# Performance work log

Measured on AMD Instinct MI355X. Metric: run time of the kernel, lower is better.

The kernel has to match this reference:

```python
import jax, jax.numpy as jnp
import numpy as np

STRIDE = (1, 1)
PADDING = ((1, 1), (1, 1))  # symmetric padding of 1 on H and W
DILATION = (1, 1)


def setup_inputs() -> dict:
    key = jax.random.key(0)
    k1, k2 = jax.random.split(key)
    x = jax.random.normal(k1, (32, 128, 56, 56), dtype=jnp.float32)
    weight = jax.random.normal(k2, (256, 128, 3, 3), dtype=jnp.float32) * 0.05
    return {"x": x, "weight": weight}


def reference(x, weight):
    # Faithful math of the im2col + matmul conv: identical to a standard
    # cross-correlation Conv2d with stride=1, padding=1, dilation=1, groups=1,
    # bias=False. Expressed as a single fused conv instead of the python-loop
    # gather + stacked GEMM of the original (same output values).
    out = jax.lax.conv_general_dilated(
        x, weight,
        window_strides=STRIDE,
        padding=PADDING,
        rhs_dilation=DILATION,
        dimension_numbers=("NCHW", "OIHW", "NCHW"),
        feature_group_count=1,
    )
    return out  # [B, C_out, H_out, W_out] = [32, 256, 56, 56]
```

## Files before the change

kernel.cpp:

```cpp
#include <hip/hip_runtime.h>
#include <stdint.h>


#define CIN   128
#define HW_   56
#define CO_   256
#define KSZ   1152
#define IMGHW 3136
#define HP    58
#define NT    18
#define XT_BYTES ((size_t)32 * HP * HP * CIN * 2)
#define WP_BYTES ((size_t)CO_ * KSZ * 2)
#define WS_NEED  (XT_BYTES + WP_BYTES)

typedef __attribute__((ext_vector_type(8))) __bf16 bf16x8;
typedef __attribute__((ext_vector_type(4))) float f32x4;
typedef __attribute__((ext_vector_type(8))) unsigned short ushort8;

__device__ __forceinline__ unsigned short f2bf(float f) {
    unsigned int u = __float_as_uint(f);
    u += 0x7fffu + ((u >> 16) & 1u);
    return (unsigned short)(u >> 16);
}

__device__ __forceinline__ void gl2lds16(const void* g, void* l) {
    __builtin_amdgcn_global_load_lds(
        (const __attribute__((address_space(1))) void*)g,
        (__attribute__((address_space(3))) void*)l, 16, 0, 0);
}

__global__ void pack_weight(const float* __restrict__ w,
                            unsigned short* __restrict__ wp) {
    int idx = blockIdx.x * 256 + threadIdx.x;
    int co = idx / KSZ;
    int k  = idx - co * KSZ;
    int khkw = k >> 7;
    int ci = k & 127;
    wp[idx] = f2bf(w[(co * CIN + ci) * 9 + khkw]);
}

__global__ __launch_bounds__(256)
void xform(const float* __restrict__ x, unsigned short* __restrict__ xt) {
    const int nb = blockIdx.x;
    const int n  = nb / HP;
    const int hp = nb - n * HP;
    unsigned short* orow = xt + ((size_t)n * HP + hp) * (HP * CIN);
    const int t = threadIdx.x;

    if (hp == 0 || hp == HP - 1) {
        for (int i = t; i < (HP * CIN) / 8; i += 256)
            ((ushort8*)orow)[i] = (ushort8){0, 0, 0, 0, 0, 0, 0, 0};
        return;
    }
    const int h = hp - 1;
    __shared__ unsigned short T[CIN][HP];
    const int wl = t & 63, cg = t >> 6;
    for (int c0 = 0; c0 < CIN; c0 += 4) {
        int ci = c0 + cg;
        if (wl < HW_)
            T[ci][wl] = f2bf(x[(((size_t)n * CIN + ci) * HW_ + h) * HW_ + wl]);
    }
    __syncthreads();
    const int ci = t & 127, wo = t >> 7;
    for (int wp_ = wo; wp_ < HP; wp_ += 2) {
        unsigned short v = 0;
        if (wp_ >= 1 && wp_ <= HW_) v = T[ci][wp_ - 1];
        orow[wp_ * CIN + ci] = v;
    }
}

__global__ __launch_bounds__(512, 1)
void conv8(const unsigned short* __restrict__ xt,
           const unsigned short* __restrict__ wpk,
           float* __restrict__ out)
{
    __shared__ __align__(16) char lds[131072];

    const int tid  = threadIdx.x;
    const int lane = tid & 63;
    const int wid  = tid >> 6;

    int bid = blockIdx.x;
    bid = (bid & 7) * 49 + (bid >> 3);
    const int m0 = bid << 8;

    const uint32_t scb = (uint32_t)((((tid & 7) ^ ((tid >> 3) & 7)) << 4));
    uint32_t aoff[4], boff[4];
    #pragma unroll
    for (int q = 0; q < 4; ++q) {
        int r = q * 64 + (tid >> 3);
        int m = m0 + r;
        int n = m / IMGHW;
        int rem = m - n * IMGHW;
        int h = rem / HW_;
        int w = rem - h * HW_;
        aoff[q] = (uint32_t)(((n * HP + h) * HP + w) << 8) + scb;
        boff[q] = (uint32_t)(r * (KSZ * 2)) + scb;
    }

    const int fr = lane & 15, fg = lane >> 4;
    const int fsw = (lane & 7) << 4;
    const int c0h = ((fg << 4)) ^ fsw;
    const int c1h = (64 | (fg << 4)) ^ fsw;
    const int wm0 = (wid >> 2) << 7;
    const int wn0 = (wid & 3) << 6;
    const int aB0 = (wm0 + fr) * 128 + c0h;
    const int aB1 = (wm0 + fr) * 128 + c1h;
    const int bB0 = 32768 + (wn0 + fr) * 128 + c0h;
    const int bB1 = 32768 + (wn0 + fr) * 128 + c1h;

    const char* xtc = (const char*)xt;
    const char* wpc = (const char*)wpk;

    f32x4 acc[8][4];
    #pragma unroll
    for (int i = 0; i < 8; ++i)
        #pragma unroll
        for (int j = 0; j < 4; ++j)
            acc[i][j] = (f32x4){0.f, 0.f, 0.f, 0.f};

    ushort8 areg[8], breg[4];

    auto STAGE = [&](int t, int q) {
        const int bufo = (t & 1) << 16;
        int tap = t >> 1;
        int kh = (tap * 11) >> 5;
        int kw = tap - kh * 3;
        uint32_t ta = aoff[q] + (uint32_t)(((kh * HP + kw) << 8) + ((t & 1) << 7));
        uint32_t tb = boff[q] + (uint32_t)(t << 7);
        char* base = &lds[bufo];
        gl2lds16(xtc + ta, base + (q << 13) + (tid << 4));
        gl2lds16(wpc + tb, base + 32768 + (q << 13) + (tid << 4));
    };

    #define LGKM0 do { asm volatile("s_waitcnt lgkmcnt(0)" ::: "memory"); \
                       __builtin_amdgcn_sched_barrier(0); } while (0)
    #define MMROW(mf) do { \
        acc[mf][0] = __builtin_amdgcn_mfma_f32_16x16x32_bf16( \
            __builtin_bit_cast(bf16x8, breg[0]), __builtin_bit_cast(bf16x8, areg[mf]), acc[mf][0], 0, 0, 0); \
        acc[mf][1] = __builtin_amdgcn_mfma_f32_16x16x32_bf16( \
            __builtin_bit_cast(bf16x8, breg[1]), __builtin_bit_cast(bf16x8, areg[mf]), acc[mf][1], 0, 0, 0); \
        acc[mf][2] = __builtin_amdgcn_mfma_f32_16x16x32_bf16( \
            __builtin_bit_cast(bf16x8, breg[2]), __builtin_bit_cast(bf16x8, areg[mf]), acc[mf][2], 0, 0, 0); \
        acc[mf][3] = __builtin_amdgcn_mfma_f32_16x16x32_bf16( \
            __builtin_bit_cast(bf16x8, breg[3]), __builtin_bit_cast(bf16x8, areg[mf]), acc[mf][3], 0, 0, 0); \
    } while (0)

    STAGE(0, 0); STAGE(0, 1); STAGE(0, 2); STAGE(0, 3);
    STAGE(1, 0);
    asm volatile("s_waitcnt vmcnt(2)" ::: "memory");
    __builtin_amdgcn_s_barrier();

    for (int t = 0; t < NT; ++t) {
        const int bufo = (t & 1) << 16;
        const char* L = lds;

        breg[0] = *(const ushort8*)(L + bufo + bB0 + 0 * 2048);
        breg[1] = *(const ushort8*)(L + bufo + bB0 + 1 * 2048);
        breg[2] = *(const ushort8*)(L + bufo + bB0 + 2 * 2048);
        breg[3] = *(const ushort8*)(L + bufo + bB0 + 3 * 2048);
        areg[0] = *(const ushort8*)(L + bufo + aB0 + 0 * 2048);
        areg[1] = *(const ushort8*)(L + bufo + aB0 + 1 * 2048);
        areg[2] = *(const ushort8*)(L + bufo + aB0 + 2 * 2048);
        areg[3] = *(const ushort8*)(L + bufo + aB0 + 3 * 2048);
        if (t + 1 < NT) STAGE(t + 1, 1);
        __builtin_amdgcn_s_barrier();
        LGKM0;
        __builtin_amdgcn_s_setprio(1);
        MMROW(0); MMROW(1); MMROW(2); MMROW(3);
        __builtin_amdgcn_s_setprio(0);
        __builtin_amdgcn_s_barrier();

        areg[4] = *(const ushort8*)(L + bufo + aB0 + 4 * 2048);
        areg[5] = *(const ushort8*)(L + bufo + aB0 + 5 * 2048);
        areg[6] = *(const ushort8*)(L + bufo + aB0 + 6 * 2048);
        areg[7] = *(const ushort8*)(L + bufo + aB0 + 7 * 2048);
        if (t + 1 < NT) STAGE(t + 1, 2);
        __builtin_amdgcn_s_barrier();
        LGKM0;
        __builtin_amdgcn_s_setprio(1);
        MMROW(4); MMROW(5); MMROW(6); MMROW(7);
        __builtin_amdgcn_s_setprio(0);
        __builtin_amdgcn_s_barrier();

        breg[0] = *(const ushort8*)(L + bufo + bB1 + 0 * 2048);
        breg[1] = *(const ushort8*)(L + bufo + bB1 + 1 * 2048);
        breg[2] = *(const ushort8*)(L + bufo + bB1 + 2 * 2048);
        breg[3] = *(const ushort8*)(L + bufo + bB1 + 3 * 2048);
        areg[0] = *(const ushort8*)(L + bufo + aB1 + 0 * 2048);
        areg[1] = *(const ushort8*)(L + bufo + aB1 + 1 * 2048);
        areg[2] = *(const ushort8*)(L + bufo + aB1 + 2 * 2048);
        areg[3] = *(const ushort8*)(L + bufo + aB1 + 3 * 2048);
        if (t + 1 < NT) STAGE(t + 1, 3);
        __builtin_amdgcn_s_barrier();
        LGKM0;
        __builtin_amdgcn_s_setprio(1);
        MMROW(0); MMROW(1); MMROW(2); MMROW(3);
        __builtin_amdgcn_s_setprio(0);
        __builtin_amdgcn_s_barrier();

        areg[4] = *(const ushort8*)(L + bufo + aB1 + 4 * 2048);
        areg[5] = *(const ushort8*)(L + bufo + aB1 + 5 * 2048);
        areg[6] = *(const ushort8*)(L + bufo + aB1 + 6 * 2048);
        areg[7] = *(const ushort8*)(L + bufo + aB1 + 7 * 2048);
        if (t + 2 < NT) STAGE(t + 2, 0);
        __builtin_amdgcn_s_barrier();
        LGKM0;
        __builtin_amdgcn_s_setprio(1);
        MMROW(4); MMROW(5); MMROW(6); MMROW(7);
        __builtin_amdgcn_s_setprio(0);
        if (t + 2 < NT)      asm volatile("s_waitcnt vmcnt(2)" ::: "memory");
        else if (t + 1 < NT) asm volatile("s_waitcnt vmcnt(0)" ::: "memory");
        __builtin_amdgcn_s_barrier();
    }

    const int mwave = m0 + wm0;
    const int co0 = wn0 + (fg << 2);
    #pragma unroll
    for (int mf = 0; mf < 8; ++mf) {
        int m = mwave + mf * 16 + fr;
        int n = m / IMGHW;
        int hwr = m - n * IMGHW;
        uint32_t basem = (uint32_t)(n * (CO_ * IMGHW) + hwr);
        #pragma unroll
        for (int nf = 0; nf < 4; ++nf)
            #pragma unroll
            for (int q = 0; q < 4; ++q)
                out[basem + (uint32_t)(co0 + nf * 16 + q) * IMGHW] = acc[mf][nf][q];
    }
    #undef LGKM0
    #undef MMROW
}

#define BM    64
#define BK    32
#define NSTEP 36
#define LDSP  40

template<bool PACKED>
__global__ __launch_bounds__(256, 2)
void conv_fb(const float* __restrict__ x,
             const float* __restrict__ wraw,
             const unsigned short* __restrict__ wp,
             float* __restrict__ out)
{
    __shared__ __align__(16) unsigned short Al[2][BM][LDSP];
    __shared__ __align__(16) unsigned short Bl[2][CO_][LDSP];

    const int tid  = threadIdx.x;
    const int lane = tid & 63;
    const int wid  = tid >> 6;

    const int mb    = blockIdx.x;
    const int n_img = mb / 49;
    const int hw0   = (mb - n_img * 49) * BM;

    const int mm = lane;
    const int hw = hw0 + mm;
    const int h  = hw / HW_;
    const int w_ = hw - h * HW_;

    const int bco  = tid >> 2;
    const int bkkg = tid & 3;

    float   aPF[8];
    ushort8 bPF[4];

    auto loadA = [&](int step) {
        int khkw = step >> 2;
        int kh = khkw / 3, kw = khkw - (khkw / 3) * 3;
        int ci0 = (step & 3) * BK + wid * 8;
        int ih = h + kh - 1, iw = w_ + kw - 1;
        bool valid = ((unsigned)ih < (unsigned)HW_) && ((unsigned)iw < (unsigned)HW_);
        const float* px = x + (((size_t)(n_img * CIN + ci0) * HW_ + ih) * HW_ + iw);
        #pragma unroll
        for (int e = 0; e < 8; ++e)
            aPF[e] = valid ? px[e * IMGHW] : 0.f;
    };
    auto writeA = [&](int buf) {
        ushort8 v;
        #pragma unroll
        for (int e = 0; e < 8; ++e) v[e] = f2bf(aPF[e]);
        *(ushort8*)&Al[buf][mm][wid * 8] = v;
    };
    auto loadB = [&](int step) {
        if (PACKED) {
            int k0 = step * BK;
            #pragma unroll
            for (int r = 0; r < 4; ++r)
                bPF[r] = *(const ushort8*)&wp[(r * 64 + bco) * KSZ + k0 + bkkg * 8];
        } else {
            int khkw = step >> 2;
            int ci0 = (step & 3) * BK + bkkg * 8;
            #pragma unroll
            for (int r = 0; r < 4; ++r) {
                int co = r * 64 + bco;
                ushort8 v;
                #pragma unroll
                for (int e = 0; e < 8; ++e)
                    v[e] = f2bf(wraw[(co * CIN + ci0 + e) * 9 + khkw]);
                bPF[r] = v;
            }
        }
    };
    auto writeB = [&](int buf) {
        #pragma unroll
        for (int r = 0; r < 4; ++r)
            *(ushort8*)&Bl[buf][r * 64 + bco][bkkg * 8] = bPF[r];
    };

    f32x4 acc[4][4];
    #pragma unroll
    for (int i = 0; i < 4; ++i)
        #pragma unroll
        for (int j = 0; j < 4; ++j)
            acc[i][j] = (f32x4){0.f, 0.f, 0.f, 0.f};

    const int frow = lane & 15;
    const int fk   = (lane >> 4) * 8;

    loadA(0); loadB(0);
    writeA(0); writeB(0);
    __syncthreads();

    for (int s = 0; s < NSTEP; ++s) {
        const int cur = s & 1;
        if (s + 1 < NSTEP) { loadA(s + 1); loadB(s + 1); }

        ushort8 aF[4], bF[4];
        #pragma unroll
        for (int i = 0; i < 4; ++i)
            aF[i] = *(const ushort8*)&Bl[cur][wid * 64 + i * 16 + frow][fk];
        #pragma unroll
        for (int j = 0; j < 4; ++j)
            bF[j] = *(const ushort8*)&Al[cur][j * 16 + frow][fk];

        #pragma unroll
        for (int i = 0; i < 4; ++i)
            #pragma unroll
            for (int j = 0; j < 4; ++j)
                acc[i][j] = __builtin_amdgcn_mfma_f32_16x16x32_bf16(
                    __builtin_bit_cast(bf16x8, aF[i]),
                    __builtin_bit_cast(bf16x8, bF[j]),
                    acc[i][j], 0, 0, 0);

        if (s + 1 < NSTEP) { writeA(cur ^ 1); writeB(cur ^ 1); }
        __syncthreads();
    }

    float* ob = out + (size_t)n_img * (CO_ * IMGHW) + hw0;
    #pragma unroll
    for (int i = 0; i < 4; ++i) {
        int co0 = wid * 64 + i * 16 + (lane >> 4) * 4;
        #pragma unroll
        for (int j = 0; j < 4; ++j) {
            int mcol = j * 16 + (lane & 15);
            #pragma unroll
            for (int q = 0; q < 4; ++q)
                ob[(size_t)(co0 + q) * IMGHW + mcol] = acc[i][j][q];
        }
    }
}

extern "C" void kernel_launch(void* const* d_in, const int* in_sizes, int n_in,
                              void* d_out, int out_size, void* d_ws, size_t ws_size,
                              hipStream_t stream) {
    (void)in_sizes; (void)n_in; (void)out_size;
    const float* x  = (const float*)d_in[0];
    const float* wt = (const float*)d_in[1];
    float* out = (float*)d_out;

    if (ws_size >= WS_NEED) {
        unsigned short* xt  = (unsigned short*)d_ws;
        unsigned short* wpk = (unsigned short*)((char*)d_ws + XT_BYTES);
        xform<<<32 * HP, 256, 0, stream>>>(x, xt);
        pack_weight<<<(CO_ * KSZ) / 256, 256, 0, stream>>>(wt, wpk);
        conv8<<<392, 512, 0, stream>>>(xt, wpk, out);
    } else if (ws_size >= WP_BYTES) {
        unsigned short* wpk = (unsigned short*)d_ws;
        pack_weight<<<(CO_ * KSZ) / 256, 256, 0, stream>>>(wt, wpk);
        conv_fb<true><<<100352 / BM, 256, 0, stream>>>(x, wt, wpk, out);
    } else {
        conv_fb<false><<<100352 / BM, 256, 0, stream>>>(x, wt, nullptr, out);
    }
}
```

Baseline: 98.77 us.

## Shrink conv M-tile to 224 rows for 448 blocks and vectorize output via LDS transpose

Reduces the per-block M tile from 256 to 224 rows, so the grid grows from 392 to 448 blocks and fills the 256 CUs more evenly (two waves instead of a partial second wave). The prefetch schedule changes: the next K step is fully staged within the current iteration and waited with vmcnt(0), dropping the two-step-ahead overlap. The epilogue now transposes accumulators through LDS scratch so each lane writes float4 stores along the spatial dimension instead of scalar strided stores. The costs are smaller MFMA reuse per block, a shallower load pipeline, and extra LDS traffic in the epilogue.

```diff
diff --git a/kernel.cpp b/kernel.cpp
--- a/kernel.cpp
+++ b/kernel.cpp
@@ -9,6 +9,10 @@
 #define IMGHW 3136
 #define HP    58
 #define NT    18
+#define BMM   224
+#define ABUF  28672
+#define BBUF  32768
+#define BUFSZ 61440
 #define XT_BYTES ((size_t)32 * HP * HP * CIN * 2)
 #define WP_BYTES ((size_t)CO_ * KSZ * 2)
 #define WS_NEED  (XT_BYTES + WP_BYTES)
@@ -74,63 +78,63 @@
            const unsigned short* __restrict__ wpk,
            float* __restrict__ out)
 {
-    __shared__ __align__(16) char lds[131072];
+    __shared__ __align__(16) char lds[2 * BUFSZ];
 
     const int tid  = threadIdx.x;
     const int lane = tid & 63;
     const int wid  = tid >> 6;
 
     int bid = blockIdx.x;
-    bid = (bid & 7) * 49 + (bid >> 3);
-    const int m0 = bid << 8;
-
-    const uint32_t scb = (uint32_t)((((tid & 7) ^ ((tid >> 3) & 7)) << 4));
+    bid = (bid & 7) * 56 + (bid >> 3);
+    const int m0 = bid * BMM;
+
+    const uint32_t scb = (uint32_t)(((tid & 7) ^ ((tid >> 3) & 7)) << 4);
     uint32_t aoff[4], boff[4];
     #pragma unroll
     for (int q = 0; q < 4; ++q) {
-        int r = q * 64 + (tid >> 3);
+        int r = 56 * q + (tid >> 3);
         int m = m0 + r;
         int n = m / IMGHW;
         int rem = m - n * IMGHW;
         int h = rem / HW_;
         int w = rem - h * HW_;
         aoff[q] = (uint32_t)(((n * HP + h) * HP + w) << 8) + scb;
-        boff[q] = (uint32_t)(r * (KSZ * 2)) + scb;
+        boff[q] = (uint32_t)((64 * q + (tid >> 3)) * (KSZ * 2)) + scb;
     }
 
     const int fr = lane & 15, fg = lane >> 4;
     const int fsw = (lane & 7) << 4;
-    const int c0h = ((fg << 4)) ^ fsw;
-    const int c1h = (64 | (fg << 4)) ^ fsw;
-    const int wm0 = (wid >> 2) << 7;
+    const int c0h = (fg << 4) ^ fsw;
+    const int c1h = ((4 | fg) << 4) ^ fsw;
+    const int wm0 = (wid >> 2) * 112;
     const int wn0 = (wid & 3) << 6;
     const int aB0 = (wm0 + fr) * 128 + c0h;
     const int aB1 = (wm0 + fr) * 128 + c1h;
-    const int bB0 = 32768 + (wn0 + fr) * 128 + c0h;
-    const int bB1 = 32768 + (wn0 + fr) * 128 + c1h;
+    const int bB0 = ABUF + (wn0 + fr) * 128 + c0h;
+    const int bB1 = ABUF + (wn0 + fr) * 128 + c1h;
 
     const char* xtc = (const char*)xt;
     const char* wpc = (const char*)wpk;
 
-    f32x4 acc[8][4];
-    #pragma unroll
-    for (int i = 0; i < 8; ++i)
+    f32x4 acc[7][4];
+    #pragma unroll
+    for (int i = 0; i < 7; ++i)
         #pragma unroll
         for (int j = 0; j < 4; ++j)
             acc[i][j] = (f32x4){0.f, 0.f, 0.f, 0.f};
 
-    ushort8 areg[8], breg[4];
+    ushort8 areg[7], breg[4];
 
     auto STAGE = [&](int t, int q) {
-        const int bufo = (t & 1) << 16;
+        const int bufo = (t & 1) * BUFSZ;
         int tap = t >> 1;
         int kh = (tap * 11) >> 5;
         int kw = tap - kh * 3;
         uint32_t ta = aoff[q] + (uint32_t)(((kh * HP + kw) << 8) + ((t & 1) << 7));
         uint32_t tb = boff[q] + (uint32_t)(t << 7);
-        char* base = &lds[bufo];
-        gl2lds16(xtc + ta, base + (q << 13) + (tid << 4));
-        gl2lds16(wpc + tb, base + 32768 + (q << 13) + (tid << 4));
+        if (tid < 448)
+            gl2lds16(xtc + ta, &lds[bufo + q * 7168 + tid * 16]);
+        gl2lds16(wpc + tb, &lds[bufo + ABUF + q * 8192 + tid * 16]);
     };
 
     #define LGKM0 do { asm volatile("s_waitcnt lgkmcnt(0)" ::: "memory"); \
@@ -147,13 +151,13 @@
     } while (0)
 
     STAGE(0, 0); STAGE(0, 1); STAGE(0, 2); STAGE(0, 3);
-    STAGE(1, 0);
-    asm volatile("s_waitcnt vmcnt(2)" ::: "memory");
+    asm volatile("s_waitcnt vmcnt(0)" ::: "memory");
     __builtin_amdgcn_s_barrier();
 
     for (int t = 0; t < NT; ++t) {
-        const int bufo = (t & 1) << 16;
+        const int bufo = (t & 1) * BUFSZ;
         const char* L = lds;
+        const bool pf = (t + 1 < NT);
 
         breg[0] = *(const ushort8*)(L + bufo + bB0 + 0 * 2048);
         breg[1] = *(const ushort8*)(L + bufo + bB0 + 1 * 2048);
@@ -163,7 +167,7 @@
         areg[1] = *(const ushort8*)(L + bufo + aB0 + 1 * 2048);
         areg[2] = *(const ushort8*)(L + bufo + aB0 + 2 * 2048);
         areg[3] = *(const ushort8*)(L + bufo + aB0 + 3 * 2048);
-        if (t + 1 < NT) STAGE(t + 1, 1);
+        if (pf) { STAGE(t + 1, 0); STAGE(t + 1, 1); }
         __builtin_amdgcn_s_barrier();
         LGKM0;
         __builtin_amdgcn_s_setprio(1);
@@ -174,12 +178,11 @@
         areg[4] = *(const ushort8*)(L + bufo + aB0 + 4 * 2048);
         areg[5] = *(const ushort8*)(L + bufo + aB0 + 5 * 2048);
         areg[6] = *(const ushort8*)(L + bufo + aB0 + 6 * 2048);
-        areg[7] = *(const ushort8*)(L + bufo + aB0 + 7 * 2048);
-        if (t + 1 < NT) STAGE(t + 1, 2);
+        if (pf) STAGE(t + 1, 2);
         __builtin_amdgcn_s_barrier();
         LGKM0;
         __builtin_amdgcn_s_setprio(1);
-        MMROW(4); MMROW(5); MMROW(6); MMROW(7);
+        MMROW(4); MMROW(5); MMROW(6);
         __builtin_amdgcn_s_setprio(0);
         __builtin_amdgcn_s_barrier();
 
@@ -191,7 +194,7 @@
         areg[1] = *(const ushort8*)(L + bufo + aB1 + 1 * 2048);
         areg[2] = *(const ushort8*)(L + bufo + aB1 + 2 * 2048);
         areg[3] = *(const ushort8*)(L + bufo + aB1 + 3 * 2048);
-        if (t + 1 < NT) STAGE(t + 1, 3);
+        if (pf) STAGE(t + 1, 3);
         __builtin_amdgcn_s_barrier();
         LGKM0;
         __builtin_amdgcn_s_setprio(1);
@@ -202,31 +205,33 @@
         areg[4] = *(const ushort8*)(L + bufo + aB1 + 4 * 2048);
         areg[5] = *(const ushort8*)(L + bufo + aB1 + 5 * 2048);
         areg[6] = *(const ushort8*)(L + bufo + aB1 + 6 * 2048);
-        areg[7] = *(const ushort8*)(L + bufo + aB1 + 7 * 2048);
-        if (t + 2 < NT) STAGE(t + 2, 0);
         __builtin_amdgcn_s_barrier();
         LGKM0;
         __builtin_amdgcn_s_setprio(1);
-        MMROW(4); MMROW(5); MMROW(6); MMROW(7);
+        MMROW(4); MMROW(5); MMROW(6);
         __builtin_amdgcn_s_setprio(0);
-        if (t + 2 < NT)      asm volatile("s_waitcnt vmcnt(2)" ::: "memory");
-        else if (t + 1 < NT) asm volatile("s_waitcnt vmcnt(0)" ::: "memory");
-        __builtin_amdgcn_s_barrier();
-    }
-
-    const int mwave = m0 + wm0;
-    const int co0 = wn0 + (fg << 2);
-    #pragma unroll
-    for (int mf = 0; mf < 8; ++mf) {
-        int m = mwave + mf * 16 + fr;
-        int n = m / IMGHW;
-        int hwr = m - n * IMGHW;
-        uint32_t basem = (uint32_t)(n * (CO_ * IMGHW) + hwr);
-        #pragma unroll
-        for (int nf = 0; nf < 4; ++nf)
+        if (pf) asm volatile("s_waitcnt vmcnt(0)" ::: "memory");
+        __builtin_amdgcn_s_barrier();
+    }
+
+    float* scr = (float*)&lds[wid * 1280];
+    const int co_l = lane >> 2;
+    const int mq4  = (lane & 3) * 4;
+    #pragma unroll
+    for (int mf = 0; mf < 7; ++mf) {
+        int ml = m0 + wm0 + mf * 16 + mq4;
+        int n = ml / IMGHW;
+        int rem = ml - n * IMGHW;
+        float* op = out + (size_t)n * (CO_ * IMGHW) + rem;
+        #pragma unroll
+        for (int nf = 0; nf < 4; ++nf) {
             #pragma unroll
             for (int q = 0; q < 4; ++q)
-                out[basem + (uint32_t)(co0 + nf * 16 + q) * IMGHW] = acc[mf][nf][q];
+                scr[(fg * 4 + q) * 20 + fr] = acc[mf][nf][q];
+            f32x4 v = *(const f32x4*)&scr[co_l * 20 + mq4];
+            int co = wn0 + nf * 16 + co_l;
+            *(f32x4*)(op + (size_t)co * IMGHW) = v;
+        }
     }
     #undef LGKM0
     #undef MMROW
@@ -375,7 +380,7 @@
         unsigned short* wpk = (unsigned short*)((char*)d_ws + XT_BYTES);
         xform<<<32 * HP, 256, 0, stream>>>(x, xt);
         pack_weight<<<(CO_ * KSZ) / 256, 256, 0, stream>>>(wt, wpk);
-        conv8<<<392, 512, 0, stream>>>(xt, wpk, out);
+        conv8<<<448, 512, 0, stream>>>(xt, wpk, out);
     } else if (ws_size >= WP_BYTES) {
         unsigned short* wpk = (unsigned short*)d_ws;
         pack_weight<<<(CO_ * KSZ) / 256, 256, 0, stream>>>(wt, wpk);
```

Measured after the change: 97.86 us. About the same (-0.9%).

## Split LDS tiles into two K-halves with 64-byte rows and narrower areg

Applied to the files above, without the earlier changes.

Reorganizes the LDS staging so each 128-wide K chunk is stored as two 64-byte-row halves with a 2-bit XOR swizzle, staged in two passes instead of four row-quarters. The A-fragment register set shrinks from 8 to 4 vectors, and loads and MFMA groups are reissued per half. The intent is to lower register pressure and change the LDS bank-conflict and prefetch pattern. The cost is a different vmcnt wait discipline and swizzle, which may add conflicts or stalls.

```diff
diff --git a/kernel.cpp b/kernel.cpp
--- a/kernel.cpp
+++ b/kernel.cpp
@@ -9,6 +9,7 @@
 #define IMGHW 3136
 #define HP    58
 #define NT    18
+#define BUFSZ 65536
 #define XT_BYTES ((size_t)32 * HP * HP * CIN * 2)
 #define WP_BYTES ((size_t)CO_ * KSZ * 2)
 #define WS_NEED  (XT_BYTES + WP_BYTES)
@@ -74,7 +75,7 @@
            const unsigned short* __restrict__ wpk,
            float* __restrict__ out)
 {
-    __shared__ __align__(16) char lds[131072];
+    __shared__ __align__(16) char lds[2 * BUFSZ];
 
     const int tid  = threadIdx.x;
     const int lane = tid & 63;
@@ -84,30 +85,26 @@
     bid = (bid & 7) * 49 + (bid >> 3);
     const int m0 = bid << 8;
 
-    const uint32_t scb = (uint32_t)((((tid & 7) ^ ((tid >> 3) & 7)) << 4));
-    uint32_t aoff[4], boff[4];
-    #pragma unroll
-    for (int q = 0; q < 4; ++q) {
-        int r = q * 64 + (tid >> 3);
+    const uint32_t scb = (uint32_t)(((tid & 3) ^ ((tid >> 3) & 3)) << 4);
+    uint32_t aoff[2], boff[2];
+    #pragma unroll
+    for (int p = 0; p < 2; ++p) {
+        int r = p * 128 + (tid >> 2);
         int m = m0 + r;
         int n = m / IMGHW;
         int rem = m - n * IMGHW;
         int h = rem / HW_;
         int w = rem - h * HW_;
-        aoff[q] = (uint32_t)(((n * HP + h) * HP + w) << 8) + scb;
-        boff[q] = (uint32_t)(r * (KSZ * 2)) + scb;
+        aoff[p] = (uint32_t)(((n * HP + h) * HP + w) << 8) + scb;
+        boff[p] = (uint32_t)(r * (KSZ * 2)) + scb;
     }
 
     const int fr = lane & 15, fg = lane >> 4;
-    const int fsw = (lane & 7) << 4;
-    const int c0h = ((fg << 4)) ^ fsw;
-    const int c1h = (64 | (fg << 4)) ^ fsw;
+    const int fswz = ((fg ^ ((fr >> 1) & 3)) << 4);
     const int wm0 = (wid >> 2) << 7;
     const int wn0 = (wid & 3) << 6;
-    const int aB0 = (wm0 + fr) * 128 + c0h;
-    const int aB1 = (wm0 + fr) * 128 + c1h;
-    const int bB0 = 32768 + (wn0 + fr) * 128 + c0h;
-    const int bB1 = 32768 + (wn0 + fr) * 128 + c1h;
+    const int aBase = (wm0 + fr) * 64 + fswz;
+    const int bBase = 32768 + (wn0 + fr) * 64 + fswz;
 
     const char* xtc = (const char*)xt;
     const char* wpc = (const char*)wpk;
@@ -119,97 +116,98 @@
         for (int j = 0; j < 4; ++j)
             acc[i][j] = (f32x4){0.f, 0.f, 0.f, 0.f};
 
-    ushort8 areg[8], breg[4];
-
-    auto STAGE = [&](int t, int q) {
-        const int bufo = (t & 1) << 16;
+    ushort8 areg[4], breg[4];
+
+    auto STAGE = [&](int t, int kh) {
+        const int bufo = (t & 1) * BUFSZ;
         int tap = t >> 1;
-        int kh = (tap * 11) >> 5;
-        int kw = tap - kh * 3;
-        uint32_t ta = aoff[q] + (uint32_t)(((kh * HP + kw) << 8) + ((t & 1) << 7));
-        uint32_t tb = boff[q] + (uint32_t)(t << 7);
-        char* base = &lds[bufo];
-        gl2lds16(xtc + ta, base + (q << 13) + (tid << 4));
-        gl2lds16(wpc + tb, base + 32768 + (q << 13) + (tid << 4));
+        int khr = (tap * 11) >> 5;
+        int kwr = tap - khr * 3;
+        uint32_t asrc = (uint32_t)(((khr * HP + kwr) << 8) + ((t & 1) << 7) + (kh << 6));
+        uint32_t bsrc = (uint32_t)((t << 7) + (kh << 6));
+        #pragma unroll
+        for (int p = 0; p < 2; ++p) {
+            gl2lds16(xtc + aoff[p] + asrc,
+                     &lds[bufo + kh * 16384 + p * 8192 + tid * 16]);
+            gl2lds16(wpc + boff[p] + bsrc,
+                     &lds[bufo + 32768 + kh * 16384 + p * 8192 + tid * 16]);
+        }
     };
 
     #define LGKM0 do { asm volatile("s_waitcnt lgkmcnt(0)" ::: "memory"); \
                        __builtin_amdgcn_sched_barrier(0); } while (0)
-    #define MMROW(mf) do { \
-        acc[mf][0] = __builtin_amdgcn_mfma_f32_16x16x32_bf16( \
-            __builtin_bit_cast(bf16x8, breg[0]), __builtin_bit_cast(bf16x8, areg[mf]), acc[mf][0], 0, 0, 0); \
-        acc[mf][1] = __builtin_amdgcn_mfma_f32_16x16x32_bf16( \
-            __builtin_bit_cast(bf16x8, breg[1]), __builtin_bit_cast(bf16x8, areg[mf]), acc[mf][1], 0, 0, 0); \
-        acc[mf][2] = __builtin_amdgcn_mfma_f32_16x16x32_bf16( \
-            __builtin_bit_cast(bf16x8, breg[2]), __builtin_bit_cast(bf16x8, areg[mf]), acc[mf][2], 0, 0, 0); \
-        acc[mf][3] = __builtin_amdgcn_mfma_f32_16x16x32_bf16( \
-            __builtin_bit_cast(bf16x8, breg[3]), __builtin_bit_cast(bf16x8, areg[mf]), acc[mf][3], 0, 0, 0); \
+    #define MM4(amf, r) do { \
+        acc[amf][0] = __builtin_amdgcn_mfma_f32_16x16x32_bf16( \
+            __builtin_bit_cast(bf16x8, breg[0]), __builtin_bit_cast(bf16x8, areg[r]), acc[amf][0], 0, 0, 0); \
+        acc[amf][1] = __builtin_amdgcn_mfma_f32_16x16x32_bf16( \
+            __builtin_bit_cast(bf16x8, breg[1]), __builtin_bit_cast(bf16x8, areg[r]), acc[amf][1], 0, 0, 0); \
+        acc[amf][2] = __builtin_amdgcn_mfma_f32_16x16x32_bf16( \
+            __builtin_bit_cast(bf16x8, breg[2]), __builtin_bit_cast(bf16x8, areg[r]), acc[amf][2], 0, 0, 0); \
+        acc[amf][3] = __builtin_amdgcn_mfma_f32_16x16x32_bf16( \
+            __builtin_bit_cast(bf16x8, breg[3]), __builtin_bit_cast(bf16x8, areg[r]), acc[amf][3], 0, 0, 0); \
     } while (0)
 
-    STAGE(0, 0); STAGE(0, 1); STAGE(0, 2); STAGE(0, 3);
-    STAGE(1, 0);
-    asm volatile("s_waitcnt vmcnt(2)" ::: "memory");
+    STAGE(0, 0); STAGE(0, 1); STAGE(1, 0);
+    asm volatile("s_waitcnt vmcnt(4)" ::: "memory");
     __builtin_amdgcn_s_barrier();
 
     for (int t = 0; t < NT; ++t) {
-        const int bufo = (t & 1) << 16;
-        const char* L = lds;
-
-        breg[0] = *(const ushort8*)(L + bufo + bB0 + 0 * 2048);
-        breg[1] = *(const ushort8*)(L + bufo + bB0 + 1 * 2048);
-        breg[2] = *(const ushort8*)(L + bufo + bB0 + 2 * 2048);
-        breg[3] = *(const ushort8*)(L + bufo + bB0 + 3 * 2048);
-        areg[0] = *(const ushort8*)(L + bufo + aB0 + 0 * 2048);
-        areg[1] = *(const ushort8*)(L + bufo + aB0 + 1 * 2048);
-        areg[2] = *(const ushort8*)(L + bufo + aB0 + 2 * 2048);
-        areg[3] = *(const ushort8*)(L + bufo + aB0 + 3 * 2048);
+        const int bufo = (t & 1) * BUFSZ;
+        const char* L = lds + bufo;
+
+        breg[0] = *(const ushort8*)(L + bBase + 0 * 1024);
+        breg[1] = *(const ushort8*)(L + bBase + 1 * 1024);
+        breg[2] = *(const ushort8*)(L + bBase + 2 * 1024);
+        breg[3] = *(const ushort8*)(L + bBase + 3 * 1024);
+        areg[0] = *(const ushort8*)(L + aBase + 0 * 1024);
+        areg[1] = *(const ushort8*)(L + aBase + 1 * 1024);
+        areg[2] = *(const ushort8*)(L + aBase + 2 * 1024);
+        areg[3] = *(const ushort8*)(L + aBase + 3 * 1024);
         if (t + 1 < NT) STAGE(t + 1, 1);
         __builtin_amdgcn_s_barrier();
         LGKM0;
         __builtin_amdgcn_s_setprio(1);
-        MMROW(0); MMROW(1); MMROW(2); MMROW(3);
+        MM4(0, 0); MM4(1, 1); MM4(2, 2); MM4(3, 3);
         __builtin_amdgcn_s_setprio(0);
         __builtin_amdgcn_s_barrier();
 
-        areg[4] = *(const ushort8*)(L + bufo + aB0 + 4 * 2048);
-        areg[5] = *(const ushort8*)(L + bufo + aB0 + 5 * 2048);
-        areg[6] = *(const ushort8*)(L + bufo + aB0 + 6 * 2048);
-        areg[7] = *(const ushort8*)(L + bufo + aB0 + 7 * 2048);
-        if (t + 1 < NT) STAGE(t + 1, 2);
+        areg[0] = *(const ushort8*)(L + aBase + 4 * 1024);
+        areg[1] = *(const ushort8*)(L + aBase + 5 * 1024);
+        areg[2] = *(const ushort8*)(L + aBase + 6 * 1024);
+        areg[3] = *(const ushort8*)(L + aBase + 7 * 1024);
         __builtin_amdgcn_s_barrier();
         LGKM0;
         __builtin_amdgcn_s_setprio(1);
-        MMROW(4); MMROW(5); MMROW(6); MMROW(7);
+        MM4(4, 0); MM4(5, 1); MM4(6, 2); MM4(7, 3);
         __builtin_amdgcn_s_setprio(0);
         __builtin_amdgcn_s_barrier();
 
-        breg[0] = *(const ushort8*)(L + bufo + bB1 + 0 * 2048);
-        breg[1] = *(const ushort8*)(L + bufo + bB1 + 1 * 2048);
-        breg[2] = *(const ushort8*)(L + bufo + bB1 + 2 * 2048);
-        breg[3] = *(const ushort8*)(L + bufo + bB1 + 3 * 2048);
-        areg[0] = *(const ushort8*)(L + bufo + aB1 + 0 * 2048);
-        areg[1] = *(const ushort8*)(L + bufo + aB1 + 1 * 2048);
-        areg[2] = *(const ushort8*)(L + bufo + aB1 + 2 * 2048);
-        areg[3] = *(const ushort8*)(L + bufo + aB1 + 3 * 2048);
-        if (t + 1 < NT) STAGE(t + 1, 3);
+        breg[0] = *(const ushort8*)(L + bBase + 16384 + 0 * 1024);
+        breg[1] = *(const ushort8*)(L + bBase + 16384 + 1 * 1024);
+        breg[2] = *(const ushort8*)(L + bBase + 16384 + 2 * 1024);
+        breg[3] = *(const ushort8*)(L + bBase + 16384 + 3 * 1024);
+        areg[0] = *(const ushort8*)(L + aBase + 16384 + 0 * 1024);
+        areg[1] = *(const ushort8*)(L + aBase + 16384 + 1 * 1024);
+        areg[2] = *(const ushort8*)(L + aBase + 16384 + 2 * 1024);
+        areg[3] = *(const ushort8*)(L + aBase + 16384 + 3 * 1024);
+        if (t + 2 < NT) STAGE(t + 2, 0);
         __builtin_amdgcn_s_barrier();
         LGKM0;
         __builtin_amdgcn_s_setprio(1);
-        MMROW(0); MMROW(1); MMROW(2); MMROW(3);
+        MM4(0, 0); MM4(1, 1); MM4(2, 2); MM4(3, 3);
         __builtin_amdgcn_s_setprio(0);
         __builtin_amdgcn_s_barrier();
 
-        areg[4] = *(const ushort8*)(L + bufo + aB1 + 4 * 2048);
-        areg[5] = *(const ushort8*)(L + bufo + aB1 + 5 * 2048);
-        areg[6] = *(const ushort8*)(L + bufo + aB1 + 6 * 2048);
-        areg[7] = *(const ushort8*)(L + bufo + aB1 + 7 * 2048);
-        if (t + 2 < NT) STAGE(t + 2, 0);
+        areg[0] = *(const ushort8*)(L + aBase + 16384 + 4 * 1024);
+        areg[1] = *(const ushort8*)(L + aBase + 16384 + 5 * 1024);
+        areg[2] = *(const ushort8*)(L + aBase + 16384 + 6 * 1024);
+        areg[3] = *(const ushort8*)(L + aBase + 16384 + 7 * 1024);
         __builtin_amdgcn_s_barrier();
         LGKM0;
         __builtin_amdgcn_s_setprio(1);
-        MMROW(4); MMROW(5); MMROW(6); MMROW(7);
+        MM4(4, 0); MM4(5, 1); MM4(6, 2); MM4(7, 3);
         __builtin_amdgcn_s_setprio(0);
-        if (t + 2 < NT)      asm volatile("s_waitcnt vmcnt(2)" ::: "memory");
+        if (t + 2 < NT)      asm volatile("s_waitcnt vmcnt(4)" ::: "memory");
         else if (t + 1 < NT) asm volatile("s_waitcnt vmcnt(0)" ::: "memory");
         __builtin_amdgcn_s_barrier();
     }
@@ -229,7 +227,7 @@
                 out[basem + (uint32_t)(co0 + nf * 16 + q) * IMGHW] = acc[mf][nf][q];
     }
     #undef LGKM0
-    #undef MMROW
+    #undef MM4
 }
 
 #define BM    64
```

Measured after the change: 102.2 us. 3.5% more time.
